# Performance work log

Measured on AMD Instinct MI355X. Metric: run time of the kernel, lower is better.

The kernel has to match this reference:

```python
import jax, jax.numpy as jnp
import numpy as np

BN_EPS = 1e-5


def setup_inputs() -> dict:
    key = jax.random.key(0)
    ks = jax.random.split(key, 6)
    B, C, N = 8, 256, 2048
    C4 = C // 4
    return {
        "x": jax.random.normal(ks[0], (B, C, N), dtype=jnp.float32),
        "wq": jax.random.normal(ks[1], (C4, C), dtype=jnp.float32) * (1.0 / np.sqrt(C)),
        "wv": jax.random.normal(ks[2], (C, C), dtype=jnp.float32) * (1.0 / np.sqrt(C)),
        "bv": jax.random.normal(ks[3], (C,), dtype=jnp.float32) * 0.02,
        "wt": jax.random.normal(ks[4], (C, C), dtype=jnp.float32) * (1.0 / np.sqrt(C)),
        "bt": jax.random.normal(ks[5], (C,), dtype=jnp.float32) * 0.02,
        "gamma": jnp.ones((C,), dtype=jnp.float32),
        "beta": jnp.zeros((C,), dtype=jnp.float32),
    }


def reference(x, wq, wv, bv, wt, bt, gamma, beta):
    # x: [B, C, N]. Conv1d(kernel=1) == per-point matmul.
    # q_conv and k_conv share the same weight in the original, so q == k.
    q = jnp.einsum('oc,bcn->bon', wq, x)            # [B, C/4, N]
    # ||q_i - q_j||_2 via the Gram identity (same math as norm of the diff tensor)
    sq = jnp.sum(q * q, axis=1)                     # [B, N]
    gram = jnp.einsum('bci,bcj->bij', q, q)         # [B, N, N]
    d2 = sq[:, :, None] - 2.0 * gram + sq[:, None, :]
    l2 = jnp.sqrt(jnp.maximum(d2, 0.0))             # [B, N, N]
    attn = jax.nn.softmax(-l2, axis=-1)             # rows = queries i
    v = jnp.einsum('oc,bcn->bon', wv, x) + bv[None, :, None]   # [B, C, N]
    # einsum('bij,bkj->bik') then permute(0,2,1) == contract j directly to [B, C, N]
    x_r = jnp.einsum('bij,bcj->bci', attn, v)       # [B, C, N]
    t = jnp.einsum('oc,bcn->bon', wt, x_r) + bt[None, :, None]
    # BatchNorm1d in training mode: batch stats over (B, N), biased variance
    mean = jnp.mean(t, axis=(0, 2), keepdims=True)
    var = jnp.mean((t - mean) ** 2, axis=(0, 2), keepdims=True)
    bn = gamma[None, :, None] * (t - mean) * jax.lax.rsqrt(var + BN_EPS) + beta[None, :, None]
    return x + jnp.maximum(bn, 0.0)
```

## Files before the change

### kernel.cpp

```cpp
#include <hip/hip_runtime.h>
#include <math.h>

#define BDIM 8
#define CDIM 256
#define C4DIM 64
#define NDIM 2048
#define LOG2E_SQ 2.0813689810056077f
#define NEG_2LOG2E_SQ -4.1627379620112154f

typedef short bf16x8 __attribute__((ext_vector_type(8)));
typedef float f32x4 __attribute__((ext_vector_type(4)));

__device__ inline unsigned cvt_pk(float lo, float hi) {
  unsigned r;
  asm("v_cvt_pk_bf16_f32 %0, %1, %2" : "=v"(r) : "v"(lo), "v"(hi));
  return r;
}
__device__ inline float bflo(unsigned u) {
  u <<= 16; float f; __builtin_memcpy(&f, &u, 4); return f;
}
__device__ inline float bfhi(unsigned u) {
  u &= 0xffff0000u; float f; __builtin_memcpy(&f, &u, 4); return f;
}

__global__ __launch_bounds__(256) void prep_kernel(const float* __restrict__ x,
                                                   const float* __restrict__ wq,
                                                   const float* __restrict__ wv,
                                                   const float* __restrict__ wt,
                                                   short* __restrict__ xT,
                                                   short* __restrict__ wqb,
                                                   short* __restrict__ wvb,
                                                   short* __restrict__ wtb,
                                                   float* __restrict__ bnsum) {
  __shared__ float tile[64][65];
  const int fb = blockIdx.x, t = threadIdx.x;
  if (fb < 1024) {
    const int b = fb >> 7, c0 = ((fb >> 5) & 3) * 64, n0 = (fb & 31) * 64;
    const int cl = t >> 2, ng = (t & 3) * 16;
#pragma unroll
    for (int kk = 0; kk < 4; ++kk) {
      float4 v = *(const float4*)&x[((size_t)(b * CDIM + c0 + cl)) * NDIM + n0 + ng + kk * 4];
      tile[cl][ng + kk * 4 + 0] = v.x; tile[cl][ng + kk * 4 + 1] = v.y;
      tile[cl][ng + kk * 4 + 2] = v.z; tile[cl][ng + kk * 4 + 3] = v.w;
    }
    __syncthreads();
    const int nl = t >> 2, cg = (t & 3) * 16;
    unsigned u[8];
#pragma unroll
    for (int e = 0; e < 8; ++e)
      u[e] = cvt_pk(tile[cg + 2 * e][nl], tile[cg + 2 * e + 1][nl]);
    short* dst = &xT[((size_t)b * NDIM + n0 + nl) * CDIM + c0 + cg];
    *(uint4*)&dst[0] = make_uint4(u[0], u[1], u[2], u[3]);
    *(uint4*)&dst[8] = make_uint4(u[4], u[5], u[6], u[7]);
  } else if (fb < 1168) {
    const int idx = ((fb - 1024) * 256 + t) * 4;
    const float* src; short* dst; int off;
    if (idx < 16384)      { src = wq; dst = wqb; off = idx; }
    else if (idx < 81920) { src = wv; dst = wvb; off = idx - 16384; }
    else                  { src = wt; dst = wtb; off = idx - 81920; }
    float4 v = *(const float4*)&src[off];
    *(uint2*)&dst[off] = make_uint2(cvt_pk(v.x, v.y), cvt_pk(v.z, v.w));
  } else {
    bnsum[t] = 0.f; bnsum[256 + t] = 0.f;
  }
}

template<bool STATS>
__device__ __forceinline__ void gemm128(const short* __restrict__ Wb,
                                        const short* __restrict__ Xt,
                                        const float* __restrict__ bias,
                                        short* __restrict__ OUT,
                                        float* __restrict__ bnsum,
                                        float* __restrict__ bnss,
                                        int b, int n0, int c0, int t) {
  const int w = t >> 6, l = t & 63, il = l & 15, g = l >> 4;
  const int wn = w & 1, wc = w >> 1;
  const size_t arow = (size_t)b * NDIM + n0 + wn * 64;
  const int ccol = c0 + wc * 64;
  f32x4 acc[4][4] = {};
#pragma unroll
  for (int ks = 0; ks < 8; ++ks) {
    const int k0 = ks * 32;
    bf16x8 af[4], bfr[4];
#pragma unroll
    for (int nt = 0; nt < 4; ++nt)
      af[nt] = *(const bf16x8*)&Xt[(arow + nt * 16 + il) * CDIM + k0 + g * 8];
#pragma unroll
    for (int ct = 0; ct < 4; ++ct)
      bfr[ct] = *(const bf16x8*)&Wb[(size_t)(ccol + ct * 16 + il) * CDIM + k0 + g * 8];
#pragma unroll
    for (int nt = 0; nt < 4; ++nt)
#pragma unroll
      for (int ct = 0; ct < 4; ++ct)
        acc[nt][ct] = __builtin_amdgcn_mfma_f32_16x16x32_bf16(af[nt], bfr[ct], acc[nt][ct], 0, 0, 0);
  }
#pragma unroll
  for (int ct = 0; ct < 4; ++ct) {
    const int c = ccol + ct * 16 + il;
    const float bs = bias[c];
    float s = 0.f, ss = 0.f;
#pragma unroll
    for (int nt = 0; nt < 4; ++nt) {
      const int n = n0 + wn * 64 + nt * 16 + g * 4;
      float y0 = acc[nt][ct][0] + bs, y1 = acc[nt][ct][1] + bs;
      float y2 = acc[nt][ct][2] + bs, y3 = acc[nt][ct][3] + bs;
      *(uint2*)&OUT[((size_t)(b * CDIM + c)) * NDIM + n] =
          make_uint2(cvt_pk(y0, y1), cvt_pk(y2, y3));
      if (STATS) {
        s += y0 + y1 + y2 + y3;
        ss += y0 * y0 + y1 * y1 + y2 * y2 + y3 * y3;
      }
    }
    if (STATS) {
      s += __shfl_xor(s, 16, 64);   s += __shfl_xor(s, 32, 64);
      ss += __shfl_xor(ss, 16, 64); ss += __shfl_xor(ss, 32, 64);
      if (l < 16) { atomicAdd(&bnsum[c], s); atomicAdd(&bnss[c], ss); }
    }
  }
}

__global__ __launch_bounds__(256) void qv_gemm(const short* __restrict__ wqb,
                                               const short* __restrict__ wvb,
                                               const short* __restrict__ xT,
                                               const float* __restrict__ bv,
                                               short* __restrict__ qT,
                                               float* __restrict__ sq2,
                                               short* __restrict__ vbf) {
  const int fb = blockIdx.x, t = threadIdx.x;
  if (fb < 256) {
    const int b = fb >> 5, c0 = ((fb >> 4) & 1) * 128, n0 = (fb & 15) * 128;
    gemm128<false>(wvb, xT, bv, vbf, nullptr, nullptr, b, n0, c0, t);
  } else {
    const int f = fb - 256;
    const int b = f >> 5, n0 = (f & 31) * 64;
    const int w = t >> 6, l = t & 63, il = l & 15, g = l >> 4;
    const int nw = n0 + w * 16;
    f32x4 acc[4] = {};
#pragma unroll
    for (int ks = 0; ks < 8; ++ks) {
      const int k0 = ks * 32;
      bf16x8 bx = *(const bf16x8*)&xT[((size_t)b * NDIM + nw + il) * CDIM + k0 + g * 8];
#pragma unroll
      for (int ot = 0; ot < 4; ++ot) {
        bf16x8 aw = *(const bf16x8*)&wqb[(size_t)(ot * 16 + il) * CDIM + k0 + g * 8];
        acc[ot] = __builtin_amdgcn_mfma_f32_16x16x32_bf16(aw, bx, acc[ot], 0, 0, 0);
      }
    }
    float sqs = 0.f;
#pragma unroll
    for (int ot = 0; ot < 4; ++ot) {
      unsigned u0 = cvt_pk(acc[ot][0], acc[ot][1]);
      unsigned u1 = cvt_pk(acc[ot][2], acc[ot][3]);
      *(uint2*)&qT[((size_t)b * NDIM + nw + il) * C4DIM + ot * 16 + g * 4] = make_uint2(u0, u1);
      float f0 = bflo(u0), f1 = bfhi(u0), f2 = bflo(u1), f3 = bfhi(u1);
      sqs += f0 * f0 + f1 * f1 + f2 * f2 + f3 * f3;
    }
    sqs += __shfl_xor(sqs, 16, 64);
    sqs += __shfl_xor(sqs, 32, 64);
    if (l < 16) sq2[(size_t)b * NDIM + nw + l] = sqs * LOG2E_SQ;
  }
}

__global__ __launch_bounds__(256) void attn_mfma(const short* __restrict__ qT,
                                                 const short* __restrict__ Vb16,
                                                 const float* __restrict__ sq2,
                                                 short* __restrict__ xrT) {
  __shared__ __align__(16) short vj[2][128 * 32];
  __shared__ __align__(16) short qj[2][32 * 64];
  __shared__ __align__(16) short wlds[2][4][16][40];

  const int bid = blockIdx.x;
  const int swz = (bid & 7) * 64 + (bid >> 3);
  const int i0    = (swz & 31) * 64;
  const int chalf = (swz >> 5) & 1;
  const int b     = swz >> 6;

  const int t = threadIdx.x;
  const int w = t >> 6, l = t & 63, il = l & 15, g = l >> 4;

  const short* qTb = qT + (size_t)b * NDIM * C4DIM;
  const short* Vbb = Vb16 + ((size_t)b * CDIM + chalf * 128) * NDIM;
  const float* sqb = sq2 + (size_t)b * NDIM;

  const int iglob = i0 + w * 16 + il;
  const bf16x8 bq0 = *(const bf16x8*)&qTb[(size_t)iglob * C4DIM + g * 8];
  const bf16x8 bq1 = *(const bf16x8*)&qTb[(size_t)iglob * C4DIM + 32 + g * 8];
  const float sqi = sqb[iglob];

  const int vcb = t >> 2, vs = t & 3;
  const int vd0 = vcb * 32 + ((vs ^ ((vcb >> 1) & 3)) << 3);
  const int vd1 = vd0 + 64 * 32;
  const int qrow = t >> 3, qslot = t & 7;
  const int qd = qrow * 64 + ((qslot ^ (qrow & 7)) << 3);

  f32x4 acc[8];
#pragma unroll
  for (int k = 0; k < 8; ++k) acc[k] = {0.f, 0.f, 0.f, 0.f};
  float sumw = 0.f;

  f32x4 sqc0, sqc1;
  {
    bf16x8 qr = *(const bf16x8*)&qTb[(size_t)qrow * C4DIM + qslot * 8];
    *(bf16x8*)&qj[0][qd] = qr;
    sqc0 = *(const f32x4*)&sqb[g * 4];
    sqc1 = *(const f32x4*)&sqb[16 + g * 4];
  }
  __syncthreads();

  const int NT = NDIM / 32;
  for (int jt = 0; jt <= NT; ++jt) {
    const int p = jt & 1;
    const bool dg = (jt < NT);
    const bool dp = (jt > 0);
    const bool nq = (jt + 1 < NT);

    bf16x8 vr0 = {}, vr1 = {}, qr = {};
    f32x4 tn0 = {}, tn1 = {};
    if (dg) {
      const int j0 = jt * 32;
      vr0 = *(const bf16x8*)&Vbb[(size_t)vcb * NDIM + j0 + vs * 8];
      vr1 = *(const bf16x8*)&Vbb[(size_t)(vcb + 64) * NDIM + j0 + vs * 8];
    }
    if (nq) {
      const int j1 = (jt + 1) * 32;
      qr  = *(const bf16x8*)&qTb[(size_t)(j1 + qrow) * C4DIM + qslot * 8];
      tn0 = *(const f32x4*)&sqb[j1 + g * 4];
      tn1 = *(const f32x4*)&sqb[j1 + 16 + g * 4];
    }

    f32x4 s0 = {0.f, 0.f, 0.f, 0.f}, s1 = {0.f, 0.f, 0.f, 0.f};
    if (dg) {
      const short* qbuf = &qj[p][0];
      {
        const int row = il;
        bf16x8 aJ0 = *(const bf16x8*)&qbuf[row * 64 + ((g ^ (il & 7)) << 3)];
        bf16x8 aJ1 = *(const bf16x8*)&qbuf[row * 64 + (((4 + g) ^ (il & 7)) << 3)];
        s0 = __builtin_amdgcn_mfma_f32_16x16x32_bf16(aJ0, bq0, s0, 0, 0, 0);
        s0 = __builtin_amdgcn_mfma_f32_16x16x32_bf16(aJ1, bq1, s0, 0, 0, 0);
      }
      {
        const int row = 16 + il;
        bf16x8 aJ0 = *(const bf16x8*)&qbuf[row * 64 + ((g ^ (il & 7)) << 3)];
        bf16x8 aJ1 = *(const bf16x8*)&qbuf[row * 64 + (((4 + g) ^ (il & 7)) << 3)];
        s1 = __builtin_amdgcn_mfma_f32_16x16x32_bf16(aJ0, bq0, s1, 0, 0, 0);
        s1 = __builtin_amdgcn_mfma_f32_16x16x32_bf16(aJ1, bq1, s1, 0, 0, 0);
      }
    }

    if (dp) {
      const int pp = p ^ 1;
      const short* vbuf = &vj[pp][0];
      const bf16x8 bw = *(const bf16x8*)&wlds[pp][w][il][g * 8];
      __builtin_amdgcn_s_setprio(1);
#pragma unroll
      for (int ctl = 0; ctl < 8; ++ctl) {
        const int lr = ctl * 16 + il;
        bf16x8 aV = *(const bf16x8*)&vbuf[lr * 32 + ((g ^ ((il >> 1) & 3)) << 3)];
        acc[ctl] = __builtin_amdgcn_mfma_f32_16x16x32_bf16(aV, bw, acc[ctl], 0, 0, 0);
      }
      __builtin_amdgcn_s_setprio(0);
    }

    if (dg) {
      float wv0[4], wv1[4];
#pragma unroll
      for (int r = 0; r < 4; ++r) {
        float e0 = fmaxf(fmaf(NEG_2LOG2E_SQ, s0[r], sqi + sqc0[r]), 0.f);
        wv0[r] = __builtin_amdgcn_exp2f(-__builtin_amdgcn_sqrtf(e0));
        sumw += wv0[r];
        float e1 = fmaxf(fmaf(NEG_2LOG2E_SQ, s1[r], sqi + sqc1[r]), 0.f);
        wv1[r] = __builtin_amdgcn_exp2f(-__builtin_amdgcn_sqrtf(e1));
        sumw += wv1[r];
      }
      *(uint2*)&wlds[p][w][il][g * 4] =
          make_uint2(cvt_pk(wv0[0], wv0[1]), cvt_pk(wv0[2], wv0[3]));
      *(uint2*)&wlds[p][w][il][16 + g * 4] =
          make_uint2(cvt_pk(wv1[0], wv1[1]), cvt_pk(wv1[2], wv1[3]));
    }

    if (dg) {
      *(bf16x8*)&vj[p][vd0] = vr0;
      *(bf16x8*)&vj[p][vd1] = vr1;
    }
    if (nq) {
      *(bf16x8*)&qj[p ^ 1][qd] = qr;
      sqc0 = tn0; sqc1 = tn1;
    }
    __syncthreads();
  }

  sumw += __shfl_xor(sumw, 16, 64);
  sumw += __shfl_xor(sumw, 32, 64);
  const float inv = 1.f / sumw;
#pragma unroll
  for (int ctl = 0; ctl < 8; ++ctl) {
    float y0 = acc[ctl][0] * inv, y1 = acc[ctl][1] * inv;
    float y2 = acc[ctl][2] * inv, y3 = acc[ctl][3] * inv;
    *(uint2*)&xrT[((size_t)b * NDIM + iglob) * CDIM + chalf * 128 + ctl * 16 + g * 4] =
        make_uint2(cvt_pk(y0, y1), cvt_pk(y2, y3));
  }
}

__global__ __launch_bounds__(256) void t_gemm(const short* __restrict__ wtb,
                                              const short* __restrict__ xrT,
                                              const float* __restrict__ bt,
                                              short* __restrict__ tbf,
                                              float* __restrict__ bnsum,
                                              float* __restrict__ bnss) {
  gemm128<true>(wtb, xrT, bt, tbf, bnsum, bnss,
                blockIdx.z, blockIdx.x * 128, blockIdx.y * 128, threadIdx.x);
}

__global__ __launch_bounds__(256) void final_kernel(const float* __restrict__ x,
                                                    const short* __restrict__ tbf,
                                                    const float* __restrict__ bnsum,
                                                    const float* __restrict__ bnss,
                                                    const float* __restrict__ gamma,
                                                    const float* __restrict__ beta,
                                                    float* __restrict__ out) {
  const size_t idx = ((size_t)blockIdx.x * 256 + threadIdx.x) << 2;
  const int c = (int)((idx >> 11) & 255);
  const float cnt = (float)(BDIM * NDIM);
  const float mean = bnsum[c] / cnt;
  const float var = fmaxf(bnss[c] / cnt - mean * mean, 0.f);
  const float sc = gamma[c] * rsqrtf(var + 1e-5f);
  const float sh = beta[c] - mean * sc;
  float4 xv = *(const float4*)&x[idx];
  uint2 tu = *(const uint2*)&tbf[idx];
  const float t0 = bflo(tu.x), t1 = bfhi(tu.x), t2 = bflo(tu.y), t3 = bfhi(tu.y);
  float4 r;
  r.x = xv.x + fmaxf(t0 * sc + sh, 0.f);
  r.y = xv.y + fmaxf(t1 * sc + sh, 0.f);
  r.z = xv.z + fmaxf(t2 * sc + sh, 0.f);
  r.w = xv.w + fmaxf(t3 * sc + sh, 0.f);
  *(float4*)&out[idx] = r;
}

extern "C" void kernel_launch(void* const* d_in, const int* in_sizes, int n_in,
                              void* d_out, int out_size, void* d_ws, size_t ws_size,
                              hipStream_t stream) {
  const float* x     = (const float*)d_in[0];
  const float* wq    = (const float*)d_in[1];
  const float* wv    = (const float*)d_in[2];
  const float* bv    = (const float*)d_in[3];
  const float* wt    = (const float*)d_in[4];
  const float* bt    = (const float*)d_in[5];
  const float* gamma = (const float*)d_in[6];
  const float* beta  = (const float*)d_in[7];
  float* out = (float*)d_out;
  char* ws = (char*)d_ws;

  short* xbT   = (short*)(ws);
  short* wqb   = (short*)(ws + ((size_t)9  << 20));
  short* wvb   = (short*)(ws + ((size_t)9  << 20) + (256 << 10));
  short* wtb   = (short*)(ws + ((size_t)9  << 20) + (512 << 10));
  short* qT    = (short*)(ws + ((size_t)10 << 20));
  float* sq2   = (float*)(ws + ((size_t)12 << 20));
  short* vbf   = (short*)(ws + ((size_t)13 << 20));
  short* xrT   = (short*)(ws + ((size_t)22 << 20));
  short* tbf   = vbf;
  float* bnsum = (float*)(ws + ((size_t)31 << 20));
  float* bnss  = bnsum + 256;

  prep_kernel<<<dim3(1169), 256, 0, stream>>>(x, wq, wv, wt, xbT, wqb, wvb, wtb, bnsum);
  qv_gemm<<<dim3(512), 256, 0, stream>>>(wqb, wvb, xbT, bv, qT, sq2, vbf);
  attn_mfma<<<dim3(512), 256, 0, stream>>>(qT, vbf, sq2, xrT);
  t_gemm<<<dim3(16, 2, 8), 256, 0, stream>>>(wtb, xrT, bt, tbf, bnsum, bnss);
  final_kernel<<<dim3(4096), 256, 0, stream>>>(x, tbf, bnsum, bnss, gamma, beta, out);
}
```

Baseline: 103.0 us.

## Merge channel halves into one 512-thread attention block; read bf16 residual

The attention kernel now runs 512-thread blocks that handle both channel halves of a 64-query tile. The distance/softmax weights for each j-tile are computed once and shared across all 256 channels, where before the two channel-half blocks each recomputed them. Row sums are combined through shared memory. Separately, prep writes a bf16 copy of x and the final kernel reads it for the residual instead of fp32 x, which cuts bytes read but lowers the residual's precision. Block count halves (256 blocks), which may reduce occupancy or latency hiding.

```diff
diff --git a/kernel.cpp b/kernel.cpp
--- a/kernel.cpp
+++ b/kernel.cpp
@@ -28,6 +28,7 @@
                                                    const float* __restrict__ wv,
                                                    const float* __restrict__ wt,
                                                    short* __restrict__ xT,
+                                                   short* __restrict__ xb,
                                                    short* __restrict__ wqb,
                                                    short* __restrict__ wvb,
                                                    short* __restrict__ wtb,
@@ -39,9 +40,11 @@
     const int cl = t >> 2, ng = (t & 3) * 16;
 #pragma unroll
     for (int kk = 0; kk < 4; ++kk) {
-      float4 v = *(const float4*)&x[((size_t)(b * CDIM + c0 + cl)) * NDIM + n0 + ng + kk * 4];
+      const size_t src = ((size_t)(b * CDIM + c0 + cl)) * NDIM + n0 + ng + kk * 4;
+      float4 v = *(const float4*)&x[src];
       tile[cl][ng + kk * 4 + 0] = v.x; tile[cl][ng + kk * 4 + 1] = v.y;
       tile[cl][ng + kk * 4 + 2] = v.z; tile[cl][ng + kk * 4 + 3] = v.w;
+      *(uint2*)&xb[src] = make_uint2(cvt_pk(v.x, v.y), cvt_pk(v.z, v.w));
     }
     __syncthreads();
     const int nl = t >> 2, cg = (t & 3) * 16;
@@ -161,35 +164,36 @@
   }
 }
 
-__global__ __launch_bounds__(256) void attn_mfma(const short* __restrict__ qT,
+__global__ __launch_bounds__(512) void attn_mfma(const short* __restrict__ qT,
                                                  const short* __restrict__ Vb16,
                                                  const float* __restrict__ sq2,
                                                  short* __restrict__ xrT) {
-  __shared__ __align__(16) short vj[2][128 * 32];
+  __shared__ __align__(16) short vj[2][256 * 32];
   __shared__ __align__(16) short qj[2][32 * 64];
   __shared__ __align__(16) short wlds[2][4][16][40];
+  __shared__ float sums_lds[8][16];
 
   const int bid = blockIdx.x;
-  const int swz = (bid & 7) * 64 + (bid >> 3);
-  const int i0    = (swz & 31) * 64;
-  const int chalf = (swz >> 5) & 1;
-  const int b     = swz >> 6;
+  const int swz = (bid & 7) * 32 + (bid >> 3);
+  const int i0 = (swz & 31) * 64;
+  const int b  = swz >> 5;
 
   const int t = threadIdx.x;
   const int w = t >> 6, l = t & 63, il = l & 15, g = l >> 4;
+  const int isub = w & 3, chalf = w >> 2;
 
   const short* qTb = qT + (size_t)b * NDIM * C4DIM;
-  const short* Vbb = Vb16 + ((size_t)b * CDIM + chalf * 128) * NDIM;
+  const short* Vbb = Vb16 + (size_t)b * CDIM * NDIM;
   const float* sqb = sq2 + (size_t)b * NDIM;
 
-  const int iglob = i0 + w * 16 + il;
+  const int iglob = i0 + isub * 16 + il;
   const bf16x8 bq0 = *(const bf16x8*)&qTb[(size_t)iglob * C4DIM + g * 8];
   const bf16x8 bq1 = *(const bf16x8*)&qTb[(size_t)iglob * C4DIM + 32 + g * 8];
   const float sqi = sqb[iglob];
 
   const int vcb = t >> 2, vs = t & 3;
   const int vd0 = vcb * 32 + ((vs ^ ((vcb >> 1) & 3)) << 3);
-  const int vd1 = vd0 + 64 * 32;
+  const int vd1 = vd0 + 128 * 32;
   const int qrow = t >> 3, qslot = t & 7;
   const int qd = qrow * 64 + ((qslot ^ (qrow & 7)) << 3);
 
@@ -198,12 +202,13 @@
   for (int k = 0; k < 8; ++k) acc[k] = {0.f, 0.f, 0.f, 0.f};
   float sumw = 0.f;
 
-  f32x4 sqc0, sqc1;
+  f32x4 sqc;
   {
-    bf16x8 qr = *(const bf16x8*)&qTb[(size_t)qrow * C4DIM + qslot * 8];
-    *(bf16x8*)&qj[0][qd] = qr;
-    sqc0 = *(const f32x4*)&sqb[g * 4];
-    sqc1 = *(const f32x4*)&sqb[16 + g * 4];
+    if (t < 256) {
+      bf16x8 qr = *(const bf16x8*)&qTb[(size_t)qrow * C4DIM + qslot * 8];
+      *(bf16x8*)&qj[0][qd] = qr;
+    }
+    sqc = *(const f32x4*)&sqb[chalf * 16 + g * 4];
   }
   __syncthreads();
 
@@ -215,46 +220,36 @@
     const bool nq = (jt + 1 < NT);
 
     bf16x8 vr0 = {}, vr1 = {}, qr = {};
-    f32x4 tn0 = {}, tn1 = {};
+    f32x4 tn = {};
     if (dg) {
       const int j0 = jt * 32;
       vr0 = *(const bf16x8*)&Vbb[(size_t)vcb * NDIM + j0 + vs * 8];
-      vr1 = *(const bf16x8*)&Vbb[(size_t)(vcb + 64) * NDIM + j0 + vs * 8];
+      vr1 = *(const bf16x8*)&Vbb[(size_t)(vcb + 128) * NDIM + j0 + vs * 8];
     }
     if (nq) {
       const int j1 = (jt + 1) * 32;
-      qr  = *(const bf16x8*)&qTb[(size_t)(j1 + qrow) * C4DIM + qslot * 8];
-      tn0 = *(const f32x4*)&sqb[j1 + g * 4];
-      tn1 = *(const f32x4*)&sqb[j1 + 16 + g * 4];
-    }
-
-    f32x4 s0 = {0.f, 0.f, 0.f, 0.f}, s1 = {0.f, 0.f, 0.f, 0.f};
+      if (t < 256) qr = *(const bf16x8*)&qTb[(size_t)(j1 + qrow) * C4DIM + qslot * 8];
+      tn = *(const f32x4*)&sqb[j1 + chalf * 16 + g * 4];
+    }
+
+    f32x4 s = {0.f, 0.f, 0.f, 0.f};
     if (dg) {
       const short* qbuf = &qj[p][0];
-      {
-        const int row = il;
-        bf16x8 aJ0 = *(const bf16x8*)&qbuf[row * 64 + ((g ^ (il & 7)) << 3)];
-        bf16x8 aJ1 = *(const bf16x8*)&qbuf[row * 64 + (((4 + g) ^ (il & 7)) << 3)];
-        s0 = __builtin_amdgcn_mfma_f32_16x16x32_bf16(aJ0, bq0, s0, 0, 0, 0);
-        s0 = __builtin_amdgcn_mfma_f32_16x16x32_bf16(aJ1, bq1, s0, 0, 0, 0);
-      }
-      {
-        const int row = 16 + il;
-        bf16x8 aJ0 = *(const bf16x8*)&qbuf[row * 64 + ((g ^ (il & 7)) << 3)];
-        bf16x8 aJ1 = *(const bf16x8*)&qbuf[row * 64 + (((4 + g) ^ (il & 7)) << 3)];
-        s1 = __builtin_amdgcn_mfma_f32_16x16x32_bf16(aJ0, bq0, s1, 0, 0, 0);
-        s1 = __builtin_amdgcn_mfma_f32_16x16x32_bf16(aJ1, bq1, s1, 0, 0, 0);
-      }
+      const int row = chalf * 16 + il;
+      bf16x8 aJ0 = *(const bf16x8*)&qbuf[row * 64 + ((g ^ (il & 7)) << 3)];
+      bf16x8 aJ1 = *(const bf16x8*)&qbuf[row * 64 + (((4 + g) ^ (il & 7)) << 3)];
+      s = __builtin_amdgcn_mfma_f32_16x16x32_bf16(aJ0, bq0, s, 0, 0, 0);
+      s = __builtin_amdgcn_mfma_f32_16x16x32_bf16(aJ1, bq1, s, 0, 0, 0);
     }
 
     if (dp) {
       const int pp = p ^ 1;
       const short* vbuf = &vj[pp][0];
-      const bf16x8 bw = *(const bf16x8*)&wlds[pp][w][il][g * 8];
+      const bf16x8 bw = *(const bf16x8*)&wlds[pp][isub][il][g * 8];
       __builtin_amdgcn_s_setprio(1);
 #pragma unroll
       for (int ctl = 0; ctl < 8; ++ctl) {
-        const int lr = ctl * 16 + il;
+        const int lr = chalf * 128 + ctl * 16 + il;
         bf16x8 aV = *(const bf16x8*)&vbuf[lr * 32 + ((g ^ ((il >> 1) & 3)) << 3)];
         acc[ctl] = __builtin_amdgcn_mfma_f32_16x16x32_bf16(aV, bw, acc[ctl], 0, 0, 0);
       }
@@ -262,20 +257,15 @@
     }
 
     if (dg) {
-      float wv0[4], wv1[4];
+      float wv[4];
 #pragma unroll
       for (int r = 0; r < 4; ++r) {
-        float e0 = fmaxf(fmaf(NEG_2LOG2E_SQ, s0[r], sqi + sqc0[r]), 0.f);
-        wv0[r] = __builtin_amdgcn_exp2f(-__builtin_amdgcn_sqrtf(e0));
-        sumw += wv0[r];
-        float e1 = fmaxf(fmaf(NEG_2LOG2E_SQ, s1[r], sqi + sqc1[r]), 0.f);
-        wv1[r] = __builtin_amdgcn_exp2f(-__builtin_amdgcn_sqrtf(e1));
-        sumw += wv1[r];
+        float e = fmaxf(fmaf(NEG_2LOG2E_SQ, s[r], sqi + sqc[r]), 0.f);
+        wv[r] = __builtin_amdgcn_exp2f(-__builtin_amdgcn_sqrtf(e));
+        sumw += wv[r];
       }
-      *(uint2*)&wlds[p][w][il][g * 4] =
-          make_uint2(cvt_pk(wv0[0], wv0[1]), cvt_pk(wv0[2], wv0[3]));
-      *(uint2*)&wlds[p][w][il][16 + g * 4] =
-          make_uint2(cvt_pk(wv1[0], wv1[1]), cvt_pk(wv1[2], wv1[3]));
+      *(uint2*)&wlds[p][isub][il][chalf * 16 + g * 4] =
+          make_uint2(cvt_pk(wv[0], wv[1]), cvt_pk(wv[2], wv[3]));
     }
 
     if (dg) {
@@ -283,15 +273,17 @@
       *(bf16x8*)&vj[p][vd1] = vr1;
     }
     if (nq) {
-      *(bf16x8*)&qj[p ^ 1][qd] = qr;
-      sqc0 = tn0; sqc1 = tn1;
+      if (t < 256) *(bf16x8*)&qj[p ^ 1][qd] = qr;
+      sqc = tn;
     }
     __syncthreads();
   }
 
   sumw += __shfl_xor(sumw, 16, 64);
   sumw += __shfl_xor(sumw, 32, 64);
-  const float inv = 1.f / sumw;
+  if (l < 16) sums_lds[w][l] = sumw;
+  __syncthreads();
+  const float inv = 1.f / (sums_lds[isub][il] + sums_lds[isub + 4][il]);
 #pragma unroll
   for (int ctl = 0; ctl < 8; ++ctl) {
     float y0 = acc[ctl][0] * inv, y1 = acc[ctl][1] * inv;
@@ -311,7 +303,7 @@
                 blockIdx.z, blockIdx.x * 128, blockIdx.y * 128, threadIdx.x);
 }
 
-__global__ __launch_bounds__(256) void final_kernel(const float* __restrict__ x,
+__global__ __launch_bounds__(256) void final_kernel(const short* __restrict__ xb,
                                                     const short* __restrict__ tbf,
                                                     const float* __restrict__ bnsum,
                                                     const float* __restrict__ bnss,
@@ -325,14 +317,14 @@
   const float var = fmaxf(bnss[c] / cnt - mean * mean, 0.f);
   const float sc = gamma[c] * rsqrtf(var + 1e-5f);
   const float sh = beta[c] - mean * sc;
-  float4 xv = *(const float4*)&x[idx];
+  uint2 xu = *(const uint2*)&xb[idx];
   uint2 tu = *(const uint2*)&tbf[idx];
   const float t0 = bflo(tu.x), t1 = bfhi(tu.x), t2 = bflo(tu.y), t3 = bfhi(tu.y);
   float4 r;
-  r.x = xv.x + fmaxf(t0 * sc + sh, 0.f);
-  r.y = xv.y + fmaxf(t1 * sc + sh, 0.f);
-  r.z = xv.z + fmaxf(t2 * sc + sh, 0.f);
-  r.w = xv.w + fmaxf(t3 * sc + sh, 0.f);
+  r.x = bflo(xu.x) + fmaxf(t0 * sc + sh, 0.f);
+  r.y = bfhi(xu.x) + fmaxf(t1 * sc + sh, 0.f);
+  r.z = bflo(xu.y) + fmaxf(t2 * sc + sh, 0.f);
+  r.w = bfhi(xu.y) + fmaxf(t3 * sc + sh, 0.f);
   *(float4*)&out[idx] = r;
 }
 
@@ -351,20 +343,21 @@
   char* ws = (char*)d_ws;
 
   short* xbT   = (short*)(ws);
-  short* wqb   = (short*)(ws + ((size_t)9  << 20));
-  short* wvb   = (short*)(ws + ((size_t)9  << 20) + (256 << 10));
-  short* wtb   = (short*)(ws + ((size_t)9  << 20) + (512 << 10));
-  short* qT    = (short*)(ws + ((size_t)10 << 20));
-  float* sq2   = (float*)(ws + ((size_t)12 << 20));
-  short* vbf   = (short*)(ws + ((size_t)13 << 20));
-  short* xrT   = (short*)(ws + ((size_t)22 << 20));
+  short* xrT   = xbT;
+  short* xb    = (short*)(ws + ((size_t)8  << 20));
+  short* wqb   = (short*)(ws + ((size_t)16 << 20));
+  short* wvb   = (short*)(ws + ((size_t)16 << 20) + (256 << 10));
+  short* wtb   = (short*)(ws + ((size_t)16 << 20) + (512 << 10));
+  short* qT    = (short*)(ws + ((size_t)17 << 20));
+  float* sq2   = (float*)(ws + ((size_t)19 << 20));
+  short* vbf   = (short*)(ws + ((size_t)20 << 20));
   short* tbf   = vbf;
-  float* bnsum = (float*)(ws + ((size_t)31 << 20));
+  float* bnsum = (float*)(ws + ((size_t)28 << 20));
   float* bnss  = bnsum + 256;
 
-  prep_kernel<<<dim3(1169), 256, 0, stream>>>(x, wq, wv, wt, xbT, wqb, wvb, wtb, bnsum);
+  prep_kernel<<<dim3(1169), 256, 0, stream>>>(x, wq, wv, wt, xbT, xb, wqb, wvb, wtb, bnsum);
   qv_gemm<<<dim3(512), 256, 0, stream>>>(wqb, wvb, xbT, bv, qT, sq2, vbf);
-  attn_mfma<<<dim3(512), 256, 0, stream>>>(qT, vbf, sq2, xrT);
+  attn_mfma<<<dim3(256), 512, 0, stream>>>(qT, vbf, sq2, xrT);
   t_gemm<<<dim3(16, 2, 8), 256, 0, stream>>>(wtb, xrT, bt, tbf, bnsum, bnss);
-  final_kernel<<<dim3(4096), 256, 0, stream>>>(x, tbf, bnsum, bnss, gamma, beta, out);
-}
+  final_kernel<<<dim3(4096), 256, 0, stream>>>(xb, tbf, bnsum, bnss, gamma, beta, out);
+}
```

After: 120.4 us. 16.9% more time.
